# Performance work log

Measured on AMD Instinct MI355X. Metric: run time of the kernel, lower is better.

## Reference

```python
import jax, jax.numpy as jnp
import numpy as np

EPS = 1e-3  # keras LayerNormalization default epsilon


def layer_norm(x, g, b):
    mu = jnp.mean(x, axis=-1, keepdims=True)
    var = jnp.mean(jnp.square(x - mu), axis=-1, keepdims=True)
    return g * (x - mu) / jnp.sqrt(var + EPS) + b


def setup_inputs() -> dict:
    key = jax.random.key(0)
    ks = jax.random.split(key, 16)
    B, S, E, H, F = 2, 4096, 512, 8, 2048
    s_e = 1.0 / np.sqrt(E)
    s_f = 1.0 / np.sqrt(F)
    inp = {
        "x": jax.random.normal(ks[0], (B, S, E), dtype=jnp.float32),
        "WQ": jax.random.normal(ks[1], (E, E), dtype=jnp.float32) * s_e,
        "bQ": jnp.zeros((E,), jnp.float32),
        "WK": jax.random.normal(ks[2], (E, E), dtype=jnp.float32) * s_e,
        "bK": jnp.zeros((E,), jnp.float32),
        "WV": jax.random.normal(ks[3], (E, E), dtype=jnp.float32) * s_e,
        "bV": jnp.zeros((E,), jnp.float32),
        "WO": jax.random.normal(ks[4], (E, E), dtype=jnp.float32) * s_e,
        "bO": jnp.zeros((E,), jnp.float32),
        "W1": jax.random.normal(ks[5], (E, F), dtype=jnp.float32) * s_e,
        "b1": jnp.zeros((F,), jnp.float32),
        "W2": jax.random.normal(ks[6], (F, E), dtype=jnp.float32) * s_f,
        "b2": jnp.zeros((E,), jnp.float32),
        "g1": jnp.ones((E,), jnp.float32),
        "beta1": jnp.zeros((E,), jnp.float32),
        "g2": jnp.ones((E,), jnp.float32),
        "beta2": jnp.zeros((E,), jnp.float32),
        "num_head": 8,
    }
    return inp


def reference(x, WQ, bQ, WK, bK, WV, bV, WO, bO, W1, b1, W2, b2,
              g1, beta1, g2, beta2, num_head):
    B, S, E = x.shape
    H = num_head
    d = E // H
    scale = jnp.sqrt(jnp.asarray(d, jnp.float32))

    q = (x @ WQ + bQ).reshape(B, S, H, d).transpose(0, 2, 1, 3)  # [B,H,S,d]
    k = (x @ WK + bK).reshape(B, S, H, d).transpose(0, 2, 1, 3)
    v = (x @ WV + bV).reshape(B, S, H, d).transpose(0, 2, 1, 3)

    score = jnp.einsum('bhqd,bhkd->bhqk', q, k) / scale  # O(S^2) materialized, as in source
    attn = jax.nn.softmax(score, axis=-1)
    zs = jnp.einsum('bhqk,bhkd->bhqd', attn, v)  # [B,H,S,d]

    # Faithful to source bug: reshape [B,H,S,d] -> [B,S,E] WITHOUT transposing back
    zs = zs.reshape(B, S, E)
    zs = zs @ WO + bO

    z = layer_norm(zs + x, g1, beta1)
    r = jax.nn.relu(z @ W1 + b1) @ W2 + b2
    r = layer_norm(r + z, g2, beta2)
    return r
```

## Files before the change

### kernel.cpp

```cpp
#include <hip/hip_runtime.h>
#include <hip/hip_bf16.h>

typedef unsigned short u16;
typedef __attribute__((ext_vector_type(8))) short bf16x8;
typedef __attribute__((ext_vector_type(4))) float f32x4;
typedef __attribute__((ext_vector_type(16))) float f32x16;

static constexpr int BB = 2;
static constexpr int SS = 4096;
static constexpr int EE = 512;
static constexpr int HH = 8;
static constexpr int DD = 64;
static constexpr int FF = 2048;
static constexpr int NR = BB * SS;
static constexpr int QS = 3 * EE;

#define QSCALE 0.18033688011112042f

__device__ __forceinline__ u16 f2bf(float f) {
  union { float f; unsigned u; } v; v.f = f;
  unsigned r = v.u + 0x7FFFu + ((v.u >> 16) & 1u);
  return (u16)(r >> 16);
}
__device__ __forceinline__ unsigned pack2(float a, float b) {
  return (unsigned)f2bf(a) | ((unsigned)f2bf(b) << 16);
}
__device__ __forceinline__ float bf2f_lo(unsigned u) {
  union { unsigned u; float f; } v; v.u = u << 16; return v.f;
}
__device__ __forceinline__ float bf2f_hi(unsigned u) {
  union { unsigned u; float f; } v; v.u = u & 0xffff0000u; return v.f;
}
__device__ __forceinline__ unsigned cvtpk(float lo, float hi) {
  unsigned r;
  asm("v_cvt_pk_bf16_f32 %0, %1, %2" : "=v"(r) : "v"(lo), "v"(hi));
  return r;
}
__device__ __forceinline__ void perm32swap(unsigned& a, unsigned& b) {
  asm("v_permlane32_swap_b32 %0, %1" : "+v"(a), "+v"(b));
}
__device__ __forceinline__ void gload_lds16(const u16* g, u16* l) {
  __builtin_amdgcn_global_load_lds(
      (const __attribute__((address_space(1))) unsigned*)g,
      (__attribute__((address_space(3))) unsigned*)l, 16, 0, 0);
}

struct TrJob { const float* W; u16* Wt; int K, N, k0, n0; };

__device__ __forceinline__ void transp_tile(const float* W, u16* Wt, int K,
                                            int N, int k0, int n0, int t) {
  __shared__ float T[64][65];
  const int tn = t & 63, tk = t >> 6;
#pragma unroll
  for (int i = 0; i < 16; ++i) {
    int kk = tk * 16 + i;
    T[kk][tn] = W[(size_t)(k0 + kk) * N + n0 + tn];
  }
  __syncthreads();
#pragma unroll
  for (int i = 0; i < 16; ++i) {
    int nn = tk * 16 + i;
    Wt[(size_t)(n0 + nn) * K + k0 + tn] = f2bf(T[tn][nn]);
  }
}

__global__ __launch_bounds__(256) void prep_all(
    const float* __restrict__ x, u16* __restrict__ xb,
    const float* __restrict__ WQ, const float* __restrict__ WK,
    const float* __restrict__ WV, const float* __restrict__ WO,
    const float* __restrict__ W1, const float* __restrict__ W2,
    u16* __restrict__ Wqkv_t, u16* __restrict__ WO_t, u16* __restrict__ W1_t,
    u16* __restrict__ W2_t, const float* __restrict__ bQ,
    const float* __restrict__ bK, const float* __restrict__ bV,
    float* __restrict__ bqkv) {
  const int bx = blockIdx.x;
  const int t = threadIdx.x;
  if (bx < 2048) {
    int i = (bx * 256 + t) * 8;
    float4 a = *(const float4*)(x + i);
    float4 b = *(const float4*)(x + i + 4);
    uint4 u;
    u.x = pack2(a.x, a.y); u.y = pack2(a.z, a.w);
    u.z = pack2(b.x, b.y); u.w = pack2(b.z, b.w);
    *(uint4*)(xb + i) = u;
    return;
  }
  int idx = bx - 2048;
  if (idx < 768) {
    TrJob j;
    if (idx < 256) {
      const float* srcs[4] = {WQ, WK, WV, WO};
      u16* dsts[4] = {Wqkv_t, Wqkv_t + 512 * 512, Wqkv_t + 1024 * 512, WO_t};
      int w = idx >> 6, l = idx & 63;
      j = {srcs[w], dsts[w], 512, 512, (l & 7) * 64, (l >> 3) * 64};
    } else if (idx < 512) {
      int l = idx - 256;
      j = {W1, W1_t, 512, 2048, (l & 7) * 64, (l >> 3) * 64};
    } else {
      int l = idx - 512;
      j = {W2, W2_t, 2048, 512, (l & 31) * 64, (l >> 5) * 64};
    }
    transp_tile(j.W, j.Wt, j.K, j.N, j.k0, j.n0, t);
    return;
  }
  for (int i = t; i < QS; i += 256)
    bqkv[i] = i < 512 ? bQ[i] : (i < 1024 ? bK[i - 512] : bV[i - 1024]);
}

__global__ __launch_bounds__(256) void transp_v(const u16* __restrict__ qkvb,
                                                u16* __restrict__ vt) {
  __shared__ u16 T[64][72];
  const int s0 = blockIdx.x * 64, c0 = blockIdx.y * 64, b = blockIdx.z;
  const int t = threadIdx.x;
#pragma unroll
  for (int i = 0; i < 2; ++i) {
    int idx = t + i * 256;
    int row = idx >> 3, c8 = idx & 7;
    *(uint4*)(&T[row][c8 * 8]) = *(const uint4*)(
        &qkvb[((size_t)b * SS + s0 + row) * QS + 1024 + c0 + c8 * 8]);
  }
  __syncthreads();
#pragma unroll
  for (int i = 0; i < 2; ++i) {
    int idx = t + i * 256;
    int c = idx >> 3, s8 = idx & 7;
    u16 tmp[8];
#pragma unroll
    for (int j = 0; j < 8; ++j) tmp[j] = T[s8 * 8 + j][c];
    *(uint4*)(&vt[((size_t)b * EE + c0 + c) * SS + s0 + s8 * 8]) =
        *(uint4*)tmp;
  }
}

template <int RELU, int OUT_BF16, int SCALEQ = 0>
__global__ __launch_bounds__(256) void gemm64(
    const u16* __restrict__ A, const u16* __restrict__ Bt,
    const float* __restrict__ bias, void* __restrict__ Cout,
    int M, int N, int K) {
  __shared__ __align__(16) u16 As[2][64 * 64];
  __shared__ __align__(16) u16 Bs[2][64 * 64];
  const int t = threadIdx.x;
  const int lane = t & 63, wid = t >> 6;
  const int lm = lane & 15, lg = lane >> 4;
  const int bm = blockIdx.x * 64, bn = blockIdx.y * 64;
  const int wr = (wid >> 1) * 32, wc = (wid & 1) * 32;
  const int sr = lane >> 3;
  const int scb = (lane & 7) ^ sr;

  f32x4 acc[2][2];
#pragma unroll
  for (int i = 0; i < 2; ++i)
#pragma unroll
    for (int j = 0; j < 2; ++j) acc[i][j] = (f32x4){0.f, 0.f, 0.f, 0.f};

  auto stage = [&](int kb, int buf) {
#pragma unroll
    for (int i = 0; i < 2; ++i) {
      int r8 = wid * 16 + i * 8;
      gload_lds16(A + (size_t)(bm + r8 + sr) * K + kb + scb * 8,
                  &As[buf][r8 * 64]);
      gload_lds16(Bt + (size_t)(bn + r8 + sr) * K + kb + scb * 8,
                  &Bs[buf][r8 * 64]);
    }
  };

  stage(0, 0);
  const int nsteps = K >> 6;
  for (int s = 0; s < nsteps; ++s) {
    const int cur = s & 1;
    __syncthreads();
    if (s + 1 < nsteps) stage((s + 1) << 6, cur ^ 1);

#pragma unroll
    for (int c = 0; c < 2; ++c) {
      bf16x8 af[2], bfr[2];
#pragma unroll
      for (int i = 0; i < 2; ++i) {
        int ar = wr + i * 16 + lm;
        af[i] = *(const bf16x8*)(
            &As[cur][ar * 64 + (((c * 4 + lg) ^ (ar & 7)) << 3)]);
        int br = wc + i * 16 + lm;
        bfr[i] = *(const bf16x8*)(
            &Bs[cur][br * 64 + (((c * 4 + lg) ^ (br & 7)) << 3)]);
      }
#pragma unroll
      for (int i = 0; i < 2; ++i)
#pragma unroll
        for (int j = 0; j < 2; ++j)
          acc[i][j] = __builtin_amdgcn_mfma_f32_16x16x32_bf16(
              af[i], bfr[j], acc[i][j], 0, 0, 0);
    }
  }

  float bi[2];
#pragma unroll
  for (int j = 0; j < 2; ++j) bi[j] = bias[bn + wc + j * 16 + lm];

#pragma unroll
  for (int i = 0; i < 2; ++i) {
#pragma unroll
    for (int j = 0; j < 2; ++j) {
      int col = bn + wc + j * 16 + lm;
#pragma unroll
      for (int r = 0; r < 4; ++r) {
        int row = bm + wr + i * 16 + lg * 4 + r;
        float vv = acc[i][j][r] + bi[j];
        if (RELU) vv = fmaxf(vv, 0.f);
        if (SCALEQ && col < 512) vv *= QSCALE;
        if (OUT_BF16)
          ((u16*)Cout)[(size_t)row * N + col] = f2bf(vv);
        else
          ((float*)Cout)[(size_t)row * N + col] = vv;
      }
    }
  }
}

__global__ __launch_bounds__(128) void attn_mfma(
    const u16* __restrict__ qkv, const u16* __restrict__ vt,
    u16* __restrict__ zs) {
  __shared__ __align__(16) u16 K_lds[2][64 * 64];
  __shared__ __align__(16) u16 V_lds[2][64 * 64];
  __shared__ float Linv[2][32];

  const int bh = blockIdx.x;
  const int qblock = blockIdx.y;
  const int b = bh >> 3, h = bh & 7;
  const int t = threadIdx.x;
  const int lane = t & 63, wid = t >> 6;
  const int q32 = lane & 31, hi = lane >> 5;
  const int qs7 = q32 & 7;
  const size_t bS = (size_t)b * SS;
  const u16* kp = qkv + 512;
  const u16* vrow = vt + ((size_t)b * EE + h * DD) * SS;
  const int qbase = qblock * 64 + wid * 32;

  bf16x8 qf[4];
  {
    const u16* qrow = qkv + (bS + qbase + q32) * QS + h * DD + hi * 8;
#pragma unroll
    for (int c = 0; c < 4; ++c) qf[c] = *(const bf16x8*)(qrow + c * 16);
  }

  const int sr = lane >> 3;
  const int scb = (lane & 7) ^ sr;

  f32x16 o0, o1;
#pragma unroll
  for (int i = 0; i < 16; ++i) { o0[i] = 0.f; o1[i] = 0.f; }
  float lsum = 0.f;

  auto stage = [&](int kt, int bufi) {
#pragma unroll
    for (int i = 0; i < 4; ++i) {
      int rbase = wid * 32 + i * 8;
      gload_lds16(kp + (bS + kt * 64 + rbase + sr) * QS + h * DD + scb * 8,
                  &K_lds[bufi][rbase * 64]);
      gload_lds16(vrow + (size_t)(rbase + sr) * SS + kt * 64 + scb * 8,
                  &V_lds[bufi][rbase * 64]);
    }
  };

  stage(0, 0);

  constexpr int NT = SS / 64;
  for (int kt = 0; kt < NT; ++kt) {
    const int cur = kt & 1;
    if (kt + 1 < NT) {
      stage(kt + 1, cur ^ 1);
      asm volatile("s_waitcnt vmcnt(8)" ::: "memory");
    } else {
      asm volatile("s_waitcnt vmcnt(0)" ::: "memory");
    }
    __builtin_amdgcn_sched_barrier(0);
    __builtin_amdgcn_s_barrier();

    float p[2][16];
#pragma unroll
    for (int blk = 0; blk < 2; ++blk) {
      f32x16 s;
#pragma unroll
      for (int i = 0; i < 16; ++i) s[i] = 0.f;
      const int krow = blk * 32 + q32;
      __builtin_amdgcn_s_setprio(1);
#pragma unroll
      for (int c = 0; c < 4; ++c) {
        bf16x8 kf = *(const bf16x8*)(
            &K_lds[cur][krow * 64 + (((2 * c + hi) ^ qs7) << 3)]);
        s = __builtin_amdgcn_mfma_f32_32x32x16_bf16(kf, qf[c], s, 0, 0, 0);
      }
      __builtin_amdgcn_s_setprio(0);
#pragma unroll
      for (int r = 0; r < 16; ++r) {
        p[blk][r] = __builtin_amdgcn_exp2f(s[r]);
        lsum += p[blk][r];
      }
    }

    __builtin_amdgcn_s_setprio(1);
#pragma unroll
    for (int kc = 0; kc < 4; ++kc) {
      const int bb = kc >> 1, rA = (kc & 1) * 8, rB = rA + 4;
      unsigned wA0 = cvtpk(p[bb][rA + 0], p[bb][rA + 1]);
      unsigned wA1 = cvtpk(p[bb][rA + 2], p[bb][rA + 3]);
      unsigned wB0 = cvtpk(p[bb][rB + 0], p[bb][rB + 1]);
      unsigned wB1 = cvtpk(p[bb][rB + 2], p[bb][rB + 3]);
      perm32swap(wA0, wB0);
      perm32swap(wA1, wB1);
      union { unsigned u[4]; bf16x8 v; } pf;
      pf.u[0] = wA0; pf.u[1] = wA1; pf.u[2] = wB0; pf.u[3] = wB1;
      bf16x8 vf0 = *(const bf16x8*)(
          &V_lds[cur][q32 * 64 + (((2 * kc + hi) ^ qs7) << 3)]);
      bf16x8 vf1 = *(const bf16x8*)(
          &V_lds[cur][(32 + q32) * 64 + (((2 * kc + hi) ^ qs7) << 3)]);
      o0 = __builtin_amdgcn_mfma_f32_32x32x16_bf16(pf.v, vf0, o0, 0, 0, 0);
      o1 = __builtin_amdgcn_mfma_f32_32x32x16_bf16(pf.v, vf1, o1, 0, 0, 0);
    }
    __builtin_amdgcn_s_setprio(0);

    asm volatile("s_waitcnt lgkmcnt(0)" ::: "memory");
    __builtin_amdgcn_s_barrier();
  }

  float fl = lsum + __shfl_xor(lsum, 32);
  if (lane < 32) Linv[wid][q32] = 1.f / fl;

#pragma unroll
  for (int reg = 0; reg < 16; ++reg) {
    int q = (reg & 3) + 8 * (reg >> 2) + 4 * hi;
    float inv = Linv[wid][q];
    int s = qbase + q;
    u16* dst = zs + ((size_t)b * SS + h * 512 + (s >> 3)) * EE + (s & 7) * 64;
    dst[q32] = f2bf(o0[reg] * inv);
    dst[32 + q32] = f2bf(o1[reg] * inv);
  }
}

template <int WF32>
__global__ __launch_bounds__(128) void add_ln_b(
    const u16* __restrict__ a, const u16* __restrict__ xres,
    const float* __restrict__ g, const float* __restrict__ beta,
    u16* __restrict__ outb, float* __restrict__ outf) {
  const int row = blockIdx.x;
  const int tid = threadIdx.x;
  uint2 av = *(const uint2*)(a + (size_t)row * EE + tid * 4);
  uint2 xv = *(const uint2*)(xres + (size_t)row * EE + tid * 4);
  float vx = bf2f_lo(av.x) + bf2f_lo(xv.x);
  float vy = bf2f_hi(av.x) + bf2f_hi(xv.x);
  float vz = bf2f_lo(av.y) + bf2f_lo(xv.y);
  float vw = bf2f_hi(av.y) + bf2f_hi(xv.y);
  float sum = vx + vy + vz + vw;
  float sq = vx * vx + vy * vy + vz * vz + vw * vw;
#pragma unroll
  for (int off = 1; off < 64; off <<= 1) {
    sum += __shfl_xor(sum, off);
    sq += __shfl_xor(sq, off);
  }
  __shared__ float s0[2], s1[2];
  int w = tid >> 6;
  if ((tid & 63) == 0) { s0[w] = sum; s1[w] = sq; }
  __syncthreads();
  sum = s0[0] + s0[1];
  sq = s1[0] + s1[1];
  float mu = sum * (1.0f / EE);
  float var = sq * (1.0f / EE) - mu * mu;
  float r = rsqrtf(var + 1e-3f);
  int c = tid * 4;
  float4 gv = *(const float4*)(g + c);
  float4 bv = *(const float4*)(beta + c);
  float o0 = gv.x * (vx - mu) * r + bv.x;
  float o1 = gv.y * (vy - mu) * r + bv.y;
  float o2 = gv.z * (vz - mu) * r + bv.z;
  float o3 = gv.w * (vw - mu) * r + bv.w;
  if (WF32) {
    float4 ov = {o0, o1, o2, o3};
    *(float4*)(outf + (size_t)row * EE + c) = ov;
  } else {
    uint2 u;
    u.x = pack2(o0, o1);
    u.y = pack2(o2, o3);
    *(uint2*)(outb + (size_t)row * EE + c) = u;
  }
}

extern "C" void kernel_launch(void* const* d_in, const int* in_sizes, int n_in,
                              void* d_out, int out_size, void* d_ws,
                              size_t ws_size, hipStream_t stream) {
  const float* x = (const float*)d_in[0];
  const float* WQ = (const float*)d_in[1];
  const float* bQ = (const float*)d_in[2];
  const float* WK = (const float*)d_in[3];
  const float* bK = (const float*)d_in[4];
  const float* WV = (const float*)d_in[5];
  const float* bV = (const float*)d_in[6];
  const float* WO = (const float*)d_in[7];
  const float* bO = (const float*)d_in[8];
  const float* W1 = (const float*)d_in[9];
  const float* b1 = (const float*)d_in[10];
  const float* W2 = (const float*)d_in[11];
  const float* b2 = (const float*)d_in[12];
  const float* g1 = (const float*)d_in[13];
  const float* be1 = (const float*)d_in[14];
  const float* g2 = (const float*)d_in[15];
  const float* be2 = (const float*)d_in[16];
  float* out = (float*)d_out;

  const size_t MB = 1u << 20;
  char* w = (char*)d_ws;
  u16* Wqkv_t = (u16*)(w + 0);
  u16* WO_t   = (u16*)(w + 2 * MB);
  u16* W1_t   = (u16*)(w + 3 * MB);
  u16* W2_t   = (u16*)(w + 5 * MB);
  float* bqkv = (float*)(w + 7 * MB);
  u16* qkvb = (u16*)(w + 8 * MB);
  u16* zsb  = (u16*)(w + 32 * MB);
  u16* zs2b = (u16*)(w + 40 * MB);
  u16* f2b  = (u16*)(w + 48 * MB);
  u16* zb   = (u16*)(w + 72 * MB);
  u16* xb   = (u16*)(w + 80 * MB);
  u16* vtb  = (u16*)(w + 88 * MB);
  u16* f1   = (u16*)(w + 8 * MB);

  dim3 blk(256);

  prep_all<<<dim3(2817), blk, 0, stream>>>(x, xb, WQ, WK, WV, WO, W1, W2,
                                           Wqkv_t, WO_t, W1_t, W2_t, bQ, bK,
                                           bV, bqkv);

  gemm64<0, 1, 1><<<dim3(128, 24), blk, 0, stream>>>(xb, Wqkv_t, bqkv, qkvb,
                                                     NR, QS, EE);
  transp_v<<<dim3(SS / 64, EE / 64, BB), blk, 0, stream>>>(qkvb, vtb);
  attn_mfma<<<dim3(BB * HH, SS / 64), dim3(128), 0, stream>>>(qkvb, vtb, zsb);
  gemm64<0, 1><<<dim3(128, 8), blk, 0, stream>>>(zsb, WO_t, bO, zs2b,
                                                 NR, EE, EE);
  add_ln_b<0><<<dim3(NR), dim3(128), 0, stream>>>(zs2b, xb, g1, be1, zb,
                                                  nullptr);
  gemm64<1, 1><<<dim3(128, 32), blk, 0, stream>>>(zb, W1_t, b1, f1,
                                                  NR, FF, EE);
  gemm64<0, 1><<<dim3(128, 8), blk, 0, stream>>>(f1, W2_t, b2, f2b,
                                                 NR, EE, FF);
  add_ln_b<1><<<dim3(NR), dim3(128), 0, stream>>>(f2b, zb, g2, be2, nullptr,
                                                  out);
}
```

Baseline: 217.1 us.

## Split attention over two key halves and add a combine kernel

Attention now splits the key sequence into two halves along a new grid dimension, doubling the block count. The K/V tiles shrink to 32 keys each, which cuts LDS use, and launch bounds target 4 blocks per SM. Each half writes unnormalized bf16 partial outputs and row sums, and a new combine kernel adds them, normalizes and writes the permuted layout. The cost is an extra launch, extra global traffic for the partials, and some precision loss from rounding the partials to bf16 before summing.

After: 216.9 us. About the same (-0.1%).

```diff
diff --git a/kernel.cpp b/kernel.cpp
--- a/kernel.cpp
+++ b/kernel.cpp
@@ -216,21 +216,24 @@
   }
 }
 
-__global__ __launch_bounds__(128) void attn_mfma(
+__global__ __launch_bounds__(128, 4) void attn_split(
     const u16* __restrict__ qkv, const u16* __restrict__ vt,
-    u16* __restrict__ zs) {
-  __shared__ __align__(16) u16 K_lds[2][64 * 64];
-  __shared__ __align__(16) u16 V_lds[2][64 * 64];
-  __shared__ float Linv[2][32];
+    u16* __restrict__ po, float* __restrict__ pl) {
+  __shared__ __align__(16) u16 K_lds[2][32 * 64];
+  __shared__ __align__(16) u16 V_lds[2][64 * 32];
 
   const int bh = blockIdx.x;
   const int qblock = blockIdx.y;
+  const int half = blockIdx.z;
+  po += (size_t)half * (9u << 19);
+  pl += (size_t)half * (1u << 18);
   const int b = bh >> 3, h = bh & 7;
   const int t = threadIdx.x;
   const int lane = t & 63, wid = t >> 6;
   const int q32 = lane & 31, hi = lane >> 5;
   const int qs7 = q32 & 7;
   const size_t bS = (size_t)b * SS;
+  const int koff0 = half * 2048;
   const u16* kp = qkv + 512;
   const u16* vrow = vt + ((size_t)b * EE + h * DD) * SS;
   const int qbase = qblock * 64 + wid * 32;
@@ -244,75 +247,81 @@
 
   const int sr = lane >> 3;
   const int scb = (lane & 7) ^ sr;
-
-  f32x16 o0, o1;
-#pragma unroll
-  for (int i = 0; i < 16; ++i) { o0[i] = 0.f; o1[i] = 0.f; }
+  const int vr = lane >> 2;
+  const int vcb = (lane & 3) ^ (vr & 3);
+
+  f32x16 o0, o1, z16;
+#pragma unroll
+  for (int i = 0; i < 16; ++i) { o0[i] = 0.f; o1[i] = 0.f; z16[i] = 0.f; }
   float lsum = 0.f;
 
   auto stage = [&](int kt, int bufi) {
 #pragma unroll
-    for (int i = 0; i < 4; ++i) {
-      int rbase = wid * 32 + i * 8;
-      gload_lds16(kp + (bS + kt * 64 + rbase + sr) * QS + h * DD + scb * 8,
-                  &K_lds[bufi][rbase * 64]);
-      gload_lds16(vrow + (size_t)(rbase + sr) * SS + kt * 64 + scb * 8,
-                  &V_lds[bufi][rbase * 64]);
+    for (int i = 0; i < 2; ++i) {
+      int rb = wid * 16 + i * 8;
+      gload_lds16(
+          kp + (bS + koff0 + kt * 32 + rb + sr) * QS + h * DD + scb * 8,
+          &K_lds[bufi][rb * 64]);
+    }
+#pragma unroll
+    for (int i = 0; i < 2; ++i) {
+      int rb = wid * 32 + i * 16;
+      gload_lds16(vrow + (size_t)(rb + vr) * SS + koff0 + kt * 32 + vcb * 8,
+                  &V_lds[bufi][rb * 32]);
     }
   };
 
   stage(0, 0);
 
-  constexpr int NT = SS / 64;
+  constexpr int NT = 2048 / 32;
   for (int kt = 0; kt < NT; ++kt) {
     const int cur = kt & 1;
     if (kt + 1 < NT) {
       stage(kt + 1, cur ^ 1);
-      asm volatile("s_waitcnt vmcnt(8)" ::: "memory");
+      asm volatile("s_waitcnt vmcnt(4)" ::: "memory");
     } else {
       asm volatile("s_waitcnt vmcnt(0)" ::: "memory");
     }
     __builtin_amdgcn_sched_barrier(0);
     __builtin_amdgcn_s_barrier();
 
-    float p[2][16];
-#pragma unroll
-    for (int blk = 0; blk < 2; ++blk) {
-      f32x16 s;
-#pragma unroll
-      for (int i = 0; i < 16; ++i) s[i] = 0.f;
-      const int krow = blk * 32 + q32;
-      __builtin_amdgcn_s_setprio(1);
-#pragma unroll
-      for (int c = 0; c < 4; ++c) {
-        bf16x8 kf = *(const bf16x8*)(
-            &K_lds[cur][krow * 64 + (((2 * c + hi) ^ qs7) << 3)]);
-        s = __builtin_amdgcn_mfma_f32_32x32x16_bf16(kf, qf[c], s, 0, 0, 0);
-      }
-      __builtin_amdgcn_s_setprio(0);
-#pragma unroll
-      for (int r = 0; r < 16; ++r) {
-        p[blk][r] = __builtin_amdgcn_exp2f(s[r]);
-        lsum += p[blk][r];
-      }
-    }
-
+    f32x16 s;
     __builtin_amdgcn_s_setprio(1);
-#pragma unroll
-    for (int kc = 0; kc < 4; ++kc) {
-      const int bb = kc >> 1, rA = (kc & 1) * 8, rB = rA + 4;
-      unsigned wA0 = cvtpk(p[bb][rA + 0], p[bb][rA + 1]);
-      unsigned wA1 = cvtpk(p[bb][rA + 2], p[bb][rA + 3]);
-      unsigned wB0 = cvtpk(p[bb][rB + 0], p[bb][rB + 1]);
-      unsigned wB1 = cvtpk(p[bb][rB + 2], p[bb][rB + 3]);
+    {
+      bf16x8 kf = *(const bf16x8*)(
+          &K_lds[cur][q32 * 64 + ((hi ^ qs7) << 3)]);
+      s = __builtin_amdgcn_mfma_f32_32x32x16_bf16(kf, qf[0], z16, 0, 0, 0);
+    }
+#pragma unroll
+    for (int c = 1; c < 4; ++c) {
+      bf16x8 kf = *(const bf16x8*)(
+          &K_lds[cur][q32 * 64 + (((2 * c + hi) ^ qs7) << 3)]);
+      s = __builtin_amdgcn_mfma_f32_32x32x16_bf16(kf, qf[c], s, 0, 0, 0);
+    }
+    __builtin_amdgcn_s_setprio(0);
+    float p[16];
+#pragma unroll
+    for (int r = 0; r < 16; ++r) {
+      p[r] = __builtin_amdgcn_exp2f(s[r]);
+      lsum += p[r];
+    }
+
+    __builtin_amdgcn_s_setprio(1);
+#pragma unroll
+    for (int kc = 0; kc < 2; ++kc) {
+      const int rA = kc * 8, rB = rA + 4;
+      unsigned wA0 = cvtpk(p[rA + 0], p[rA + 1]);
+      unsigned wA1 = cvtpk(p[rA + 2], p[rA + 3]);
+      unsigned wB0 = cvtpk(p[rB + 0], p[rB + 1]);
+      unsigned wB1 = cvtpk(p[rB + 2], p[rB + 3]);
       perm32swap(wA0, wB0);
       perm32swap(wA1, wB1);
       union { unsigned u[4]; bf16x8 v; } pf;
       pf.u[0] = wA0; pf.u[1] = wA1; pf.u[2] = wB0; pf.u[3] = wB1;
       bf16x8 vf0 = *(const bf16x8*)(
-          &V_lds[cur][q32 * 64 + (((2 * kc + hi) ^ qs7) << 3)]);
+          &V_lds[cur][q32 * 32 + (((2 * kc + hi) ^ (q32 & 3)) << 3)]);
       bf16x8 vf1 = *(const bf16x8*)(
-          &V_lds[cur][(32 + q32) * 64 + (((2 * kc + hi) ^ qs7) << 3)]);
+          &V_lds[cur][(32 + q32) * 32 + (((2 * kc + hi) ^ (q32 & 3)) << 3)]);
       o0 = __builtin_amdgcn_mfma_f32_32x32x16_bf16(pf.v, vf0, o0, 0, 0, 0);
       o1 = __builtin_amdgcn_mfma_f32_32x32x16_bf16(pf.v, vf1, o1, 0, 0, 0);
     }
@@ -323,17 +332,39 @@
   }
 
   float fl = lsum + __shfl_xor(lsum, 32);
-  if (lane < 32) Linv[wid][q32] = 1.f / fl;
-
+  const size_t rowbase = (size_t)bh * 4096 + qbase;
+  if (lane < 32) pl[rowbase + q32] = fl;
 #pragma unroll
   for (int reg = 0; reg < 16; ++reg) {
     int q = (reg & 3) + 8 * (reg >> 2) + 4 * hi;
-    float inv = Linv[wid][q];
-    int s = qbase + q;
-    u16* dst = zs + ((size_t)b * SS + h * 512 + (s >> 3)) * EE + (s & 7) * 64;
-    dst[q32] = f2bf(o0[reg] * inv);
-    dst[32 + q32] = f2bf(o1[reg] * inv);
-  }
+    u16* dst = po + (rowbase + q) * 64;
+    dst[q32] = f2bf(o0[reg]);
+    dst[32 + q32] = f2bf(o1[reg]);
+  }
+}
+
+__global__ __launch_bounds__(256) void attn_combine(
+    const u16* __restrict__ po0, const u16* __restrict__ po1,
+    const float* __restrict__ pl0, const float* __restrict__ pl1,
+    u16* __restrict__ zs) {
+  const int row = blockIdx.x * 32 + (threadIdx.x >> 3);
+  const int dblk = (threadIdx.x & 7) * 8;
+  const int bh = row >> 12, s = row & 4095;
+  const int b = bh >> 3, h = bh & 7;
+  const float inv = 1.f / (pl0[row] + pl1[row]);
+  uint4 a = *(const uint4*)(po0 + (size_t)row * 64 + dblk);
+  uint4 c = *(const uint4*)(po1 + (size_t)row * 64 + dblk);
+  uint4 r;
+  r.x = pack2((bf2f_lo(a.x) + bf2f_lo(c.x)) * inv,
+              (bf2f_hi(a.x) + bf2f_hi(c.x)) * inv);
+  r.y = pack2((bf2f_lo(a.y) + bf2f_lo(c.y)) * inv,
+              (bf2f_hi(a.y) + bf2f_hi(c.y)) * inv);
+  r.z = pack2((bf2f_lo(a.z) + bf2f_lo(c.z)) * inv,
+              (bf2f_hi(a.z) + bf2f_hi(c.z)) * inv);
+  r.w = pack2((bf2f_lo(a.w) + bf2f_lo(c.w)) * inv,
+              (bf2f_hi(a.w) + bf2f_hi(c.w)) * inv);
+  u16* dst = zs + ((size_t)b * SS + h * 512 + (s >> 3)) * EE + (s & 7) * 64;
+  *(uint4*)(dst + dblk) = r;
 }
 
 template <int WF32>
@@ -414,8 +445,12 @@
   float* bqkv = (float*)(w + 7 * MB);
   u16* qkvb = (u16*)(w + 8 * MB);
   u16* zsb  = (u16*)(w + 32 * MB);
+  u16* po0  = (u16*)(w + 40 * MB);
+  u16* po1  = (u16*)(w + 49 * MB);
+  float* pl0 = (float*)(w + 58 * MB);
+  float* pl1 = (float*)(w + 59 * MB);
   u16* zs2b = (u16*)(w + 40 * MB);
-  u16* f2b  = (u16*)(w + 48 * MB);
+  u16* f2b  = (u16*)(w + 49 * MB);
   u16* zb   = (u16*)(w + 72 * MB);
   u16* xb   = (u16*)(w + 80 * MB);
   u16* vtb  = (u16*)(w + 88 * MB);
@@ -426,11 +461,12 @@
   prep_all<<<dim3(2817), blk, 0, stream>>>(x, xb, WQ, WK, WV, WO, W1, W2,
                                            Wqkv_t, WO_t, W1_t, W2_t, bQ, bK,
                                            bV, bqkv);
-
   gemm64<0, 1, 1><<<dim3(128, 24), blk, 0, stream>>>(xb, Wqkv_t, bqkv, qkvb,
                                                      NR, QS, EE);
   transp_v<<<dim3(SS / 64, EE / 64, BB), blk, 0, stream>>>(qkvb, vtb);
-  attn_mfma<<<dim3(BB * HH, SS / 64), dim3(128), 0, stream>>>(qkvb, vtb, zsb);
+  attn_split<<<dim3(BB * HH, SS / 64, 2), dim3(128), 0, stream>>>(qkvb, vtb,
+                                                                  po0, pl0);
+  attn_combine<<<dim3(2048), blk, 0, stream>>>(po0, po1, pl0, pl1, zsb);
   gemm64<0, 1><<<dim3(128, 8), blk, 0, stream>>>(zsb, WO_t, bO, zs2b,
                                                  NR, EE, EE);
   add_ln_b<0><<<dim3(NR), dim3(128), 0, stream>>>(zs2b, xb, g1, be1, zb,
```
